# Kernel optimization log

Hardware: AMD Instinct MI355X
Metric: run time of the kernel (lower is better)

Reference implementation:

```python
import jax, jax.numpy as jnp
import numpy as np

B, T, C, H = 8, 2048, 1024, 64

def setup_inputs() -> dict:
    key = jax.random.key(0)
    kx, kq, kk, kv = jax.random.split(key, 4)
    scale = 1.0 / np.sqrt(C)
    return {
        "x": jax.random.normal(kx, (B, T, C), dtype=jnp.float32),
        "Wq": jax.random.normal(kq, (C, H), dtype=jnp.float32) * scale,
        "Wk": jax.random.normal(kk, (C, H), dtype=jnp.float32) * scale,
        "Wv": jax.random.normal(kv, (C, H), dtype=jnp.float32) * scale,
    }

def reference(x, Wq, Wk, Wv):
    # q,k,v: [B,T,H]
    q = jnp.einsum('btc,ch->bth', x, Wq)
    k = jnp.einsum('btc,ch->bth', x, Wk)
    v = jnp.einsum('btc,ch->bth', x, Wv)
    scale = k.shape[-1] ** -0.5
    wei = jnp.einsum('bth,bsh->bts', q, k) * scale  # [B,T,T]
    causal = jnp.tril(jnp.ones((x.shape[1], x.shape[1]), dtype=bool))
    wei = jnp.where(causal, wei, -jnp.inf)
    wei = jax.nn.softmax(wei, axis=-1)
    out = jnp.einsum('bts,bsh->bth', wei, v)  # [B,T,H]
    return out
```

## Files before the change

### kernel.cpp

```cpp
#include <hip/hip_runtime.h>

#define B_ 8
#define T_ 2048
#define C_ 1024
#define H_ 64

typedef __bf16 bf16x8 __attribute__((ext_vector_type(8)));
typedef float  f32x4  __attribute__((ext_vector_type(4)));
typedef unsigned short u16x8 __attribute__((ext_vector_type(8)));

__device__ __forceinline__ unsigned short f2bf(float f) {
    unsigned u = __builtin_bit_cast(unsigned, f);
    u += 0x8000u;
    return (unsigned short)(u >> 16);
}

__device__ __forceinline__ float bf2f(unsigned short v) {
    unsigned u = ((unsigned)v) << 16;
    return __builtin_bit_cast(float, u);
}

__device__ __forceinline__ unsigned pack2(float lo, float hi) {
    unsigned a = __builtin_bit_cast(unsigned, lo) + 0x8000u;
    unsigned b = __builtin_bit_cast(unsigned, hi) + 0x8000u;
    return (a >> 16) | (b & 0xffff0000u);
}

union U8 { unsigned u32[4]; u16x8 v; };

__device__ __forceinline__ u16x8 cvt8(float4 f0, float4 f1) {
    U8 r;
    r.u32[0] = pack2(f0.x, f0.y);
    r.u32[1] = pack2(f0.z, f0.w);
    r.u32[2] = pack2(f1.x, f1.y);
    r.u32[3] = pack2(f1.z, f1.w);
    return r.v;
}

__device__ __forceinline__ bf16x8 load8_bf(const unsigned short* p) {
    return __builtin_bit_cast(bf16x8, *(const u16x8*)p);
}


__global__ void cast_weights(const float* __restrict__ Wq,
                             const float* __restrict__ Wk,
                             const float* __restrict__ Wv,
                             unsigned short* __restrict__ Wtf) {
    int idx = blockIdx.x * blockDim.x + threadIdx.x;
    int n   = idx % 192;
    int c   = idx / 192;
    int w   = n >> 6;
    int h   = n & 63;
    const float* W = (w == 0) ? Wq : (w == 1) ? Wk : Wv;
    int nt = n >> 4, l16 = n & 15;
    int kk = c >> 5, quad = (c >> 3) & 3, j = c & 7;
    Wtf[(size_t)(nt * 32 + kk) * 512 + l16 * 32 + quad * 8 + j] =
        f2bf(W[(size_t)c * H_ + h]);
}

__global__ __launch_bounds__(256) void qkv_proj(
        const float* __restrict__ x,
        const unsigned short* __restrict__ Wtf,
        unsigned short* __restrict__ Qf,
        unsigned short* __restrict__ Kf,
        unsigned short* __restrict__ Vf) {
    __shared__ __attribute__((aligned(16))) unsigned short As_[32 * 512];

    const int tid  = threadIdx.x;
    const int ns   = tid >> 6;
    const int lane = tid & 63;
    const int l16  = lane & 15;
    const int quad = lane >> 4;
    const size_t r0 = (size_t)blockIdx.x * 32;
    const int bb    = (int)(r0 >> 11);
    const int tloc0 = (int)(r0 & (T_ - 1));
    const int t16_0 = tloc0 >> 4;
    const int s32   = tloc0 >> 5;

    f32x4 acc[6];
#pragma unroll
    for (int i = 0; i < 6; i++) acc[i] = (f32x4){0.f, 0.f, 0.f, 0.f};

    const int sw   = l16 & 7;
    const int loff = l16 * 32 + quad * 8;

    for (int p = 0; p < 2; p++) {
        if (p) __syncthreads();
#pragma unroll
        for (int i = 0; i < 8; i++) {
            int c   = i * 256 + tid;
            int row = c >> 6;
            int g   = c & 63;
            const float* sp = x + (r0 + row) * C_ + p * 512 + g * 8;
            float4 f0 = *(const float4*)sp;
            float4 f1 = *(const float4*)(sp + 4);
            int off = row * 512 + ((g & ~7) + ((g & 7) ^ (row & 7))) * 8;
            *(u16x8*)(&As_[off]) = cvt8(f0, f1);
        }
        __syncthreads();

#pragma unroll 4
        for (int kc = 0; kc < 16; kc++) {
            int g  = kc * 4 + quad;
            int gs = ((g & ~7) + ((g & 7) ^ sw)) * 8;
            bf16x8 a0 = load8_bf(&As_[l16 * 512 + gs]);
            bf16x8 a1 = load8_bf(&As_[(16 + l16) * 512 + gs]);
            int kk = p * 16 + kc;
#pragma unroll
            for (int i = 0; i < 3; i++) {
                bf16x8 b = load8_bf(Wtf + (size_t)((ns * 3 + i) * 32 + kk) * 512 + loff);
                acc[i]     = __builtin_amdgcn_mfma_f32_16x16x32_bf16(a0, b, acc[i],     0, 0, 0);
                acc[3 + i] = __builtin_amdgcn_mfma_f32_16x16x32_bf16(a1, b, acc[3 + i], 0, 0, 0);
            }
        }
    }

    __syncthreads();
    unsigned short* E = As_;
#pragma unroll
    for (int i = 0; i < 3; i++) {
        int nt = ns * 3 + i;
#pragma unroll
        for (int msI = 0; msI < 2; msI++) {
#pragma unroll
            for (int r = 0; r < 4; r++) {
                unsigned short bv = f2bf(acc[msI * 3 + i][r]);
                int off;
                int ch;
                if (nt < 4) {
                    ch  = msI * 2 + (nt >> 1);
                    off = (quad * 4 + r) * 32 + ((nt & 1) * 2 + (l16 >> 3)) * 8 + (l16 & 7);
                } else if (nt < 8) {
                    int nk = nt - 4;
                    ch  = 4 + msI * 2 + (nk >> 1);
                    off = (quad * 4 + r) * 32 + ((nk & 1) * 2 + (l16 >> 3)) * 8 + (l16 & 7);
                } else {
                    int w32 = msI * 16 + quad * 4 + r;
                    ch  = 8 + (nt - 8);
                    off = l16 * 32 + (w32 >> 3) * 8 + (w32 & 7);
                }
                E[ch * 512 + off] = bv;
            }
        }
    }
    __syncthreads();

#pragma unroll
    for (int i = 0; i < 3; i++) {
        int gi = i * 256 + tid;
        int ch = gi >> 6;
        int g  = gi & 63;
        unsigned short* dst;
        if (ch < 4) {
            dst = Qf + ((size_t)(bb * 128 + t16_0 + (ch >> 1)) * 2 + (ch & 1)) * 512;
        } else if (ch < 8) {
            int c2 = ch - 4;
            dst = Kf + ((size_t)(bb * 128 + t16_0 + (c2 >> 1)) * 2 + (c2 & 1)) * 512;
        } else {
            dst = Vf + ((size_t)(bb * 64 + s32) * 4 + (ch - 8)) * 512;
        }
        *(u16x8*)(dst + g * 8) = *(const u16x8*)(&E[ch * 512 + g * 8]);
    }
}

#define PROW 33
#define OMS2 66

__global__ __launch_bounds__(256) void attn(
        const unsigned short* __restrict__ Qf,
        const unsigned short* __restrict__ Kf,
        const unsigned short* __restrict__ Vf,
        float* __restrict__ out) {
    __shared__ unsigned int ps_[4 * 32 * PROW];
    __shared__ unsigned short Om_[4 * 32 * OMS2];
    __shared__ float mred_[4][32];
    __shared__ float lred_[4][32];

    const int tid  = threadIdx.x;
    const int wave = tid >> 6;
    const int lane = tid & 63;
    const int l16  = lane & 15;
    const int quad = lane >> 4;
    const int b    = blockIdx.x & 7;
    const int qt32 = blockIdx.x >> 3;
    const int q0   = qt32 * 32;
    const int tdiag = qt32 >> 1;

    const int loff = l16 * 32 + quad * 8;

    bf16x8 qf[2][2];
#pragma unroll
    for (int qg = 0; qg < 2; qg++) {
        const unsigned short* Qfb = Qf + (size_t)((b * 128 + qt32 * 2 + qg) * 2) * 512;
        qf[qg][0] = load8_bf(Qfb + loff);
        qf[qg][1] = load8_bf(Qfb + 512 + loff);
    }

    f32x4 o[8];
#pragma unroll
    for (int i = 0; i < 8; i++) o[i] = (f32x4){0.f, 0.f, 0.f, 0.f};
    float m_run[2] = {-1e30f, -1e30f}, l_run[2] = {0.f, 0.f};

    const float scale = 0.125f;
    const unsigned short* Kfb = Kf + (size_t)b * 128 * 1024;
    const unsigned short* Vfb = Vf + (size_t)b * 64 * 2048;
    unsigned int* Pw = &ps_[wave * 32 * PROW];

    for (int t = wave; t <= tdiag; t += 4) {
        bf16x8 vf[8];
#pragma unroll
        for (int ks = 0; ks < 2; ks++)
#pragma unroll
            for (int ht = 0; ht < 4; ht++)
                vf[ht * 2 + ks] = load8_bf(
                    Vfb + ((size_t)(t * 2 + ks) * 4 + ht) * 512 + loff);

        f32x4 s[2][4];
#pragma unroll
        for (int nt = 0; nt < 4; nt++) {
            const unsigned short* kp = Kfb + (size_t)(t * 4 + nt) * 1024;
            bf16x8 kf0 = load8_bf(kp + loff);
            bf16x8 kf1 = load8_bf(kp + 512 + loff);
#pragma unroll
            for (int qg = 0; qg < 2; qg++) {
                f32x4 z = (f32x4){0.f, 0.f, 0.f, 0.f};
                z = __builtin_amdgcn_mfma_f32_16x16x32_bf16(kf0, qf[qg][0], z, 0, 0, 0);
                z = __builtin_amdgcn_mfma_f32_16x16x32_bf16(kf1, qf[qg][1], z, 0, 0, 0);
                s[qg][nt] = z;
            }
        }

#pragma unroll
        for (int qg = 0; qg < 2; qg++)
#pragma unroll
            for (int nt = 0; nt < 4; nt++)
#pragma unroll
                for (int r = 0; r < 4; r++) s[qg][nt][r] *= scale;

        if (t == tdiag) {
#pragma unroll
            for (int qg = 0; qg < 2; qg++) {
                int q = q0 + qg * 16 + l16;
#pragma unroll
                for (int nt = 0; nt < 4; nt++)
#pragma unroll
                    for (int r = 0; r < 4; r++) {
                        int key = t * 64 + nt * 16 + quad * 4 + r;
                        if (key > q) s[qg][nt][r] = -1e30f;
                    }
            }
        }

#pragma unroll
        for (int qg = 0; qg < 2; qg++) {
            float m0 = fmaxf(fmaxf(s[qg][0][0], s[qg][0][1]), fmaxf(s[qg][0][2], s[qg][0][3]));
            float m1 = fmaxf(fmaxf(s[qg][1][0], s[qg][1][1]), fmaxf(s[qg][1][2], s[qg][1][3]));
            float m2 = fmaxf(fmaxf(s[qg][2][0], s[qg][2][1]), fmaxf(s[qg][2][2], s[qg][2][3]));
            float m3 = fmaxf(fmaxf(s[qg][3][0], s[qg][3][1]), fmaxf(s[qg][3][2], s[qg][3][3]));
            float mx = fmaxf(fmaxf(m0, m1), fmaxf(m2, m3));
            mx = fmaxf(mx, __shfl_xor(mx, 16));
            mx = fmaxf(mx, __shfl_xor(mx, 32));
            const float m_new = fmaxf(m_run[qg], mx);
            const float alpha = __expf(m_run[qg] - m_new);
            m_run[qg] = m_new;

            float rs = 0.f;
#pragma unroll
            for (int nt = 0; nt < 4; nt++) {
#pragma unroll
                for (int i = 0; i < 2; i++) {
                    float p0 = __expf(s[qg][nt][2 * i]     - m_new);
                    float p1 = __expf(s[qg][nt][2 * i + 1] - m_new);
                    rs += p0 + p1;
                    Pw[(qg * 16 + l16) * PROW + nt * 8 + quad * 2 + i] = pack2(p0, p1);
                }
            }
            rs += __shfl_xor(rs, 16);
            rs += __shfl_xor(rs, 32);
            l_run[qg] = l_run[qg] * alpha + rs;

#pragma unroll
            for (int ht = 0; ht < 4; ht++)
#pragma unroll
                for (int r = 0; r < 4; r++) o[qg * 4 + ht][r] *= alpha;
        }

#pragma unroll
        for (int ks = 0; ks < 2; ks++) {
#pragma unroll
            for (int qg = 0; qg < 2; qg++) {
                bf16x8 pB = __builtin_bit_cast(bf16x8,
                    *(const u16x8*)(&Pw[(qg * 16 + l16) * PROW + ks * 16 + quad * 4]));
#pragma unroll
                for (int ht = 0; ht < 4; ht++)
                    o[qg * 4 + ht] = __builtin_amdgcn_mfma_f32_16x16x32_bf16(
                        vf[ht * 2 + ks], pB, o[qg * 4 + ht], 0, 0, 0);
            }
        }
    }

#pragma unroll
    for (int qg = 0; qg < 2; qg++) {
#pragma unroll
        for (int ht = 0; ht < 4; ht++)
#pragma unroll
            for (int r = 0; r < 4; r++)
                Om_[(wave * 32 + qg * 16 + l16) * OMS2 + ht * 16 + quad * 4 + r] =
                    f2bf(o[qg * 4 + ht][r]);
        if (quad == 0) {
            mred_[wave][qg * 16 + l16] = m_run[qg];
            lred_[wave][qg * 16 + l16] = l_run[qg];
        }
    }
    __syncthreads();

    const int hcol = tid & 63;
    const int qr0  = tid >> 6;
#pragma unroll
    for (int qq = 0; qq < 8; qq++) {
        const int q = qr0 + qq * 4;
        float M = -1e30f;
#pragma unroll
        for (int w = 0; w < 4; w++) M = fmaxf(M, mred_[w][q]);
        float lt = 0.f, ov = 0.f;
#pragma unroll
        for (int w = 0; w < 4; w++) {
            float e = __expf(mred_[w][q] - M);
            lt += e * lred_[w][q];
            ov += e * bf2f(Om_[(w * 32 + q) * OMS2 + hcol]);
        }
        out[((size_t)b * T_ + q0 + q) * H_ + hcol] = ov / lt;
    }
}

extern "C" void kernel_launch(void* const* d_in, const int* in_sizes, int n_in,
                              void* d_out, int out_size, void* d_ws, size_t ws_size,
                              hipStream_t stream) {
    const float* x  = (const float*)d_in[0];
    const float* Wq = (const float*)d_in[1];
    const float* Wk = (const float*)d_in[2];
    const float* Wv = (const float*)d_in[3];
    float* out = (float*)d_out;

    unsigned short* Qf  = (unsigned short*)d_ws;
    unsigned short* Kf  = Qf + (size_t)B_ * T_ * H_;
    unsigned short* Vf  = Kf + (size_t)B_ * T_ * H_;
    unsigned short* Wtf = Vf + (size_t)B_ * T_ * H_;

    cast_weights<<<(192 * C_) / 256, 256, 0, stream>>>(Wq, Wk, Wv, Wtf);
    qkv_proj<<<B_ * T_ / 32, 256, 0, stream>>>(x, Wtf, Qf, Kf, Vf);
    attn<<<B_ * (T_ / 32), 256, 0, stream>>>(Qf, Kf, Vf, out);
}
```

Before: 141.4 us.

## Double-buffer QKV projection tiles in LDS and split N across two blocks

Rewrites the QKV projection to stage both x and weight tiles through double-buffered shared memory in 64-wide K steps. The next step's global loads are issued before the current step's MFMAs, so memory latency is meant to overlap with compute. The 192 output columns are split across two blocks per 32-row tile, doubling grid size for occupancy. The cost is that each x tile is loaded and converted twice, and there is a barrier every K step. The weight cast now writes a plain transposed layout.

```diff
diff --git a/kernel.cpp b/kernel.cpp
--- a/kernel.cpp
+++ b/kernel.cpp
@@ -45,73 +45,100 @@
 __global__ void cast_weights(const float* __restrict__ Wq,
                              const float* __restrict__ Wk,
                              const float* __restrict__ Wv,
-                             unsigned short* __restrict__ Wtf) {
+                             unsigned short* __restrict__ Wt) {
     int idx = blockIdx.x * blockDim.x + threadIdx.x;
-    int n   = idx % 192;
-    int c   = idx / 192;
-    int w   = n >> 6;
-    int h   = n & 63;
+    int w   = idx >> 16;
+    int rem = idx & 0xffff;
+    int c   = rem & (C_ - 1);
+    int h   = rem >> 10;
     const float* W = (w == 0) ? Wq : (w == 1) ? Wk : Wv;
-    int nt = n >> 4, l16 = n & 15;
-    int kk = c >> 5, quad = (c >> 3) & 3, j = c & 7;
-    Wtf[(size_t)(nt * 32 + kk) * 512 + l16 * 32 + quad * 8 + j] =
-        f2bf(W[(size_t)c * H_ + h]);
-}
+    Wt[(size_t)(w * H_ + h) * C_ + c] = f2bf(W[(size_t)c * H_ + h]);
+}
+
+#define ABUF 2048
+#define BBUF 6144
 
 __global__ __launch_bounds__(256) void qkv_proj(
         const float* __restrict__ x,
-        const unsigned short* __restrict__ Wtf,
+        const unsigned short* __restrict__ Wt,
         unsigned short* __restrict__ Qf,
         unsigned short* __restrict__ Kf,
         unsigned short* __restrict__ Vf) {
-    __shared__ __attribute__((aligned(16))) unsigned short As_[32 * 512];
+    __shared__ __attribute__((aligned(16))) unsigned short As_[2 * ABUF];
+    __shared__ __attribute__((aligned(16))) unsigned short Bs_[2 * BBUF];
 
     const int tid  = threadIdx.x;
-    const int ns   = tid >> 6;
+    const int wave = tid >> 6;
     const int lane = tid & 63;
     const int l16  = lane & 15;
     const int quad = lane >> 4;
-    const size_t r0 = (size_t)blockIdx.x * 32;
+    const int ms   = wave >> 1;
+    const int nsub = wave & 1;
+    const int mb   = blockIdx.x >> 1;
+    const int nh   = blockIdx.x & 1;
+    const size_t r0 = (size_t)mb * 32;
     const int bb    = (int)(r0 >> 11);
     const int tloc0 = (int)(r0 & (T_ - 1));
     const int t16_0 = tloc0 >> 4;
-    const int s32   = tloc0 >> 5;
-
-    f32x4 acc[6];
-#pragma unroll
-    for (int i = 0; i < 6; i++) acc[i] = (f32x4){0.f, 0.f, 0.f, 0.f};
-
-    const int sw   = l16 & 7;
-    const int loff = l16 * 32 + quad * 8;
-
-    for (int p = 0; p < 2; p++) {
-        if (p) __syncthreads();
-#pragma unroll
-        for (int i = 0; i < 8; i++) {
-            int c   = i * 256 + tid;
-            int row = c >> 6;
-            int g   = c & 63;
-            const float* sp = x + (r0 + row) * C_ + p * 512 + g * 8;
-            float4 f0 = *(const float4*)sp;
-            float4 f1 = *(const float4*)(sp + 4);
-            int off = row * 512 + ((g & ~7) + ((g & 7) ^ (row & 7))) * 8;
-            *(u16x8*)(&As_[off]) = cvt8(f0, f1);
-        }
-        __syncthreads();
-
-#pragma unroll 4
-        for (int kc = 0; kc < 16; kc++) {
-            int g  = kc * 4 + quad;
-            int gs = ((g & ~7) + ((g & 7) ^ sw)) * 8;
-            bf16x8 a0 = load8_bf(&As_[l16 * 512 + gs]);
-            bf16x8 a1 = load8_bf(&As_[(16 + l16) * 512 + gs]);
-            int kk = p * 16 + kc;
-#pragma unroll
-            for (int i = 0; i < 3; i++) {
-                bf16x8 b = load8_bf(Wtf + (size_t)((ns * 3 + i) * 32 + kk) * 512 + loff);
-                acc[i]     = __builtin_amdgcn_mfma_f32_16x16x32_bf16(a0, b, acc[i],     0, 0, 0);
-                acc[3 + i] = __builtin_amdgcn_mfma_f32_16x16x32_bf16(a1, b, acc[3 + i], 0, 0, 0);
-            }
+    const int s32_0 = tloc0 >> 5;
+
+    const int srow = tid >> 3, sg = tid & 7;
+    const float* sa_src = x + (r0 + srow) * C_ + sg * 8;
+    const unsigned short* wb = Wt + (size_t)(nh * 96) * C_;
+    const int a_off = srow * 64 + ((sg ^ (srow & 7)) * 8);
+
+    f32x4 acc[3];
+#pragma unroll
+    for (int i = 0; i < 3; i++) acc[i] = (f32x4){0.f, 0.f, 0.f, 0.f};
+
+    const int sw = l16 & 7;
+
+    {
+        float4 f0 = *(const float4*)(sa_src);
+        float4 f1 = *(const float4*)(sa_src + 4);
+        *(u16x8*)(&As_[a_off]) = cvt8(f0, f1);
+#pragma unroll
+        for (int p = 0; p < 3; p++) {
+            u16x8 v = *(const u16x8*)(wb + (size_t)(p * 32 + srow) * C_ + sg * 8);
+            *(u16x8*)(&Bs_[p * 2048 + a_off]) = v;
+        }
+    }
+    __syncthreads();
+
+    int cur = 0;
+    for (int ks = 0; ks < 16; ks++) {
+        const int k1 = (ks + 1) * 64;
+        const bool more = (k1 < C_);
+        float4 na0, na1;
+        u16x8 nb0, nb1, nb2;
+        if (more) {
+            na0 = *(const float4*)(sa_src + k1);
+            na1 = *(const float4*)(sa_src + k1 + 4);
+            nb0 = *(const u16x8*)(wb + (size_t)(0 * 32 + srow) * C_ + k1 + sg * 8);
+            nb1 = *(const u16x8*)(wb + (size_t)(1 * 32 + srow) * C_ + k1 + sg * 8);
+            nb2 = *(const u16x8*)(wb + (size_t)(2 * 32 + srow) * C_ + k1 + sg * 8);
+        }
+        const unsigned short* Ac = As_ + cur * ABUF;
+        const unsigned short* Bc = Bs_ + cur * BBUF;
+        const int arow = ms * 16 + l16;
+        bf16x8 a0 = load8_bf(&Ac[arow * 64 + ((quad ^ sw) * 8)]);
+        bf16x8 a1 = load8_bf(&Ac[arow * 64 + (((quad + 4) ^ sw) * 8)]);
+#pragma unroll
+        for (int i = 0; i < 3; i++) {
+            int brow = (nsub * 3 + i) * 16 + l16;
+            bf16x8 b0 = load8_bf(&Bc[brow * 64 + ((quad ^ sw) * 8)]);
+            bf16x8 b1 = load8_bf(&Bc[brow * 64 + (((quad + 4) ^ sw) * 8)]);
+            acc[i] = __builtin_amdgcn_mfma_f32_16x16x32_bf16(a0, b0, acc[i], 0, 0, 0);
+            acc[i] = __builtin_amdgcn_mfma_f32_16x16x32_bf16(a1, b1, acc[i], 0, 0, 0);
+        }
+        if (more) {
+            const int nxt = cur ^ 1;
+            *(u16x8*)(&As_[nxt * ABUF + a_off]) = cvt8(na0, na1);
+            *(u16x8*)(&Bs_[nxt * BBUF + 0 * 2048 + a_off]) = nb0;
+            *(u16x8*)(&Bs_[nxt * BBUF + 1 * 2048 + a_off]) = nb1;
+            *(u16x8*)(&Bs_[nxt * BBUF + 2 * 2048 + a_off]) = nb2;
+            __syncthreads();
+            cur = nxt;
         }
     }
 
@@ -119,47 +146,44 @@
     unsigned short* E = As_;
 #pragma unroll
     for (int i = 0; i < 3; i++) {
-        int nt = ns * 3 + i;
-#pragma unroll
-        for (int msI = 0; msI < 2; msI++) {
-#pragma unroll
-            for (int r = 0; r < 4; r++) {
-                unsigned short bv = f2bf(acc[msI * 3 + i][r]);
-                int off;
-                int ch;
-                if (nt < 4) {
-                    ch  = msI * 2 + (nt >> 1);
-                    off = (quad * 4 + r) * 32 + ((nt & 1) * 2 + (l16 >> 3)) * 8 + (l16 & 7);
-                } else if (nt < 8) {
-                    int nk = nt - 4;
-                    ch  = 4 + msI * 2 + (nk >> 1);
-                    off = (quad * 4 + r) * 32 + ((nk & 1) * 2 + (l16 >> 3)) * 8 + (l16 & 7);
-                } else {
-                    int w32 = msI * 16 + quad * 4 + r;
-                    ch  = 8 + (nt - 8);
-                    off = l16 * 32 + (w32 >> 3) * 8 + (w32 & 7);
-                }
-                E[ch * 512 + off] = bv;
-            }
+        int nt = nh * 6 + nsub * 3 + i;
+#pragma unroll
+        for (int r = 0; r < 4; r++) {
+            unsigned short bv = f2bf(acc[i][r]);
+            int ch, off;
+            if (nt < 4) {
+                ch  = ms * 2 + (nt >> 1);
+                off = (quad * 4 + r) * 32 + ((nt & 1) * 2 + (l16 >> 3)) * 8 + (l16 & 7);
+            } else if (nt < 8) {
+                int nk = nt - 4;
+                ch  = (nh == 0) ? (4 + ms) : ms;
+                off = (quad * 4 + r) * 32 + ((nk & 1) * 2 + (l16 >> 3)) * 8 + (l16 & 7);
+            } else {
+                int w32 = ms * 16 + quad * 4 + r;
+                ch  = 2 + (nt - 8);
+                off = l16 * 32 + (w32 >> 3) * 8 + (w32 & 7);
+            }
+            E[ch * 512 + off] = bv;
         }
     }
     __syncthreads();
 
 #pragma unroll
-    for (int i = 0; i < 3; i++) {
-        int gi = i * 256 + tid;
-        int ch = gi >> 6;
-        int g  = gi & 63;
-        unsigned short* dst;
-        if (ch < 4) {
-            dst = Qf + ((size_t)(bb * 128 + t16_0 + (ch >> 1)) * 2 + (ch & 1)) * 512;
-        } else if (ch < 8) {
-            int c2 = ch - 4;
-            dst = Kf + ((size_t)(bb * 128 + t16_0 + (c2 >> 1)) * 2 + (c2 & 1)) * 512;
-        } else {
-            dst = Vf + ((size_t)(bb * 64 + s32) * 4 + (ch - 8)) * 512;
-        }
-        *(u16x8*)(dst + g * 8) = *(const u16x8*)(&E[ch * 512 + g * 8]);
+    for (int it = 0; it < 2; it++) {
+        int gi = it * 256 + tid;
+        if (gi < 384) {
+            int ch = gi >> 6;
+            int g  = gi & 63;
+            unsigned short* dst;
+            if (nh == 0) {
+                if (ch < 4) dst = Qf + ((size_t)(bb * 128 + t16_0 + (ch >> 1)) * 2 + (ch & 1)) * 512;
+                else        dst = Kf + ((size_t)(bb * 128 + t16_0 + (ch - 4)) * 2 + 0) * 512;
+            } else {
+                if (ch < 2) dst = Kf + ((size_t)(bb * 128 + t16_0 + ch) * 2 + 1) * 512;
+                else        dst = Vf + ((size_t)(bb * 64 + s32_0) * 4 + (ch - 2)) * 512;
+            }
+            *(u16x8*)(dst + g * 8) = *(const u16x8*)(&E[ch * 512 + g * 8]);
+        }
     }
 }
 
@@ -342,12 +366,12 @@
     const float* Wv = (const float*)d_in[3];
     float* out = (float*)d_out;
 
-    unsigned short* Qf  = (unsigned short*)d_ws;
-    unsigned short* Kf  = Qf + (size_t)B_ * T_ * H_;
-    unsigned short* Vf  = Kf + (size_t)B_ * T_ * H_;
-    unsigned short* Wtf = Vf + (size_t)B_ * T_ * H_;
-
-    cast_weights<<<(192 * C_) / 256, 256, 0, stream>>>(Wq, Wk, Wv, Wtf);
-    qkv_proj<<<B_ * T_ / 32, 256, 0, stream>>>(x, Wtf, Qf, Kf, Vf);
+    unsigned short* Qf = (unsigned short*)d_ws;
+    unsigned short* Kf = Qf + (size_t)B_ * T_ * H_;
+    unsigned short* Vf = Kf + (size_t)B_ * T_ * H_;
+    unsigned short* Wt = Vf + (size_t)B_ * T_ * H_;
+
+    cast_weights<<<(3 * C_ * H_) / 256, 256, 0, stream>>>(Wq, Wk, Wv, Wt);
+    qkv_proj<<<(B_ * T_ / 32) * 2, 256, 0, stream>>>(x, Wt, Qf, Kf, Vf);
     attn<<<B_ * (T_ / 32), 256, 0, stream>>>(Qf, Kf, Vf, out);
 }
```

New measurement: 141.4 us. Within noise of the previous version (+0.0%).
